# Optimization experiments

Hardware: AMD Instinct MI355X
Metric: run time of the kernel (lower is better)

The kernel has to match this reference:

```python
import jax, jax.numpy as jnp
import numpy as np

N_NODES = 50000
N_EDGES = 800000
N_GRAPHS = 128
IN_CH = 31
HID = 64
EPS = 1e-5


def _glorot(key, shape, scale=0.05):
    return jax.random.normal(key, shape, dtype=jnp.float32) * scale


def setup_inputs() -> dict:
    key = jax.random.key(0)
    ks = jax.random.split(key, 16)
    x = jax.random.normal(ks[0], (N_NODES, IN_CH), dtype=jnp.float32)
    edge_index = jax.random.randint(ks[1], (2, N_EDGES), 0, N_NODES, dtype=jnp.int32)
    batch = jnp.sort(jax.random.randint(ks[2], (N_NODES,), 0, N_GRAPHS, dtype=jnp.int32))
    params = {
        "t": jnp.ones((1,), dtype=jnp.float32),  # shared learnable softmax temperature
        "W1r": _glorot(ks[3], (HID, IN_CH)), "b1": jnp.zeros((HID,), jnp.float32), "W1s": _glorot(ks[4], (HID, IN_CH)),
        "W2r": _glorot(ks[5], (HID, HID)),  "b2": jnp.zeros((HID,), jnp.float32), "W2s": _glorot(ks[6], (HID, HID)),
        "W3r": _glorot(ks[7], (HID, HID)),  "b3": jnp.zeros((HID,), jnp.float32), "W3s": _glorot(ks[8], (HID, HID)),
        "Wl1": _glorot(ks[9], (2 * HID, 3 * HID)), "bl1": jnp.zeros((2 * HID,), jnp.float32),
        "Wl2": _glorot(ks[10], (HID // 2, 2 * HID)), "bl2": jnp.zeros((HID // 2,), jnp.float32),
    }
    return {"x": x, "edge_index": edge_index, "batch": batch, **params}


def _softmax_aggr(m, dst, t, n):
    # segment-softmax over incoming edges, per channel: alpha = softmax(t*m | dst)
    logits = m * t  # [E, C]
    mx = jax.ops.segment_max(logits, dst, num_segments=n)  # [N, C]
    e = jnp.exp(logits - mx[dst])
    denom = jax.ops.segment_sum(e, dst, num_segments=n)
    alpha = e / denom[dst]
    return jax.ops.segment_sum(m * alpha, dst, num_segments=n)  # [N, C]


def _graph_conv(x, src, dst, t, Wr, br, Ws):
    # PyG GraphConv: out = lin_rel(aggr_j x_j) + lin_root(x); lin_root has no bias
    m = x[src]  # gather [E, C]
    aggr = _softmax_aggr(m, dst, t, x.shape[0])
    return aggr @ Wr.T + br + x @ Ws.T


def _instance_norm(x):
    # torch InstanceNorm1d on [N, C] input -> normalize each row over feature dim
    mu = jnp.mean(x, axis=1, keepdims=True)
    var = jnp.mean((x - mu) ** 2, axis=1, keepdims=True)
    return (x - mu) / jnp.sqrt(var + EPS)


def reference(x, edge_index, batch, t, W1r, b1, W1s, W2r, b2, W2s, W3r, b3, W3s, Wl1, bl1, Wl2, bl2):
    src, dst = edge_index[0], edge_index[1]
    x1 = jax.nn.relu(_instance_norm(_graph_conv(x, src, dst, t, W1r, b1, W1s)))
    x2 = jax.nn.relu(_instance_norm(_graph_conv(x1, src, dst, t, W2r, b2, W2s)))
    x3 = jax.nn.relu(_instance_norm(_graph_conv(x2, src, dst, t, W3r, b3, W3s)))
    h1 = jax.ops.segment_max(x1, batch, num_segments=N_GRAPHS)
    h2 = jax.ops.segment_max(x2, batch, num_segments=N_GRAPHS)
    h3 = jax.ops.segment_max(x3, batch, num_segments=N_GRAPHS)
    h = jnp.concatenate([h1, h2, h3], axis=1)  # [G, 3*HID]
    z = jax.nn.relu(h @ Wl1.T + bl1)  # dropout is identity in eval mode
    z = z @ Wl2.T + bl2
    norm = jnp.maximum(jnp.linalg.norm(z, axis=1, keepdims=True), 1e-12)
    return z / norm
```

## Files before the change

kernel.cpp:

```cpp
#include <hip/hip_runtime.h>
#include <hip/hip_fp16.h>

#define N_NODES 50000
#define N_EDGES 800000
#define N_GRAPHS 128
#define IN_CH 31
#define HID 64

typedef __attribute__((ext_vector_type(8))) short short8;
typedef __attribute__((ext_vector_type(8))) unsigned short ushort8;
typedef __attribute__((ext_vector_type(4))) float floatx4;
typedef __attribute__((ext_vector_type(8))) _Float16 half8;
typedef __attribute__((ext_vector_type(2))) _Float16 half2v;

#if __has_builtin(__builtin_amdgcn_fdot2)
#define HAS_FDOT2 1
#endif

__device__ inline unsigned short f2h(float f) {
    __half h = __float2half_rn(f);
    return __half_as_ushort(h);
}
__device__ inline unsigned packh2(float a, float b) {
    __half2 h = __floats2half2_rn(a, b);
    return *(unsigned*)&h;
}
__device__ inline void pack4h(short* p, float4 v) {
    unsigned lo = packh2(v.x, v.y);
    unsigned hi = packh2(v.z, v.w);
    *(uint2*)p = make_uint2(lo, hi);
}
__device__ inline unsigned packEP(float E, float P) {
    return packh2(E, P);
}
__device__ inline float2 unpackEP(unsigned u) {
    __half2 h = *(__half2*)&u;
    return __half22float2(h);
}
__device__ inline half2v u2h2(unsigned u) {
    return __builtin_bit_cast(half2v, u);
}

__global__ void prep_kernel(const float* __restrict__ x, const float* __restrict__ tptr,
                            unsigned short* __restrict__ xh, unsigned* __restrict__ EP0,
                            int nN) {
    int i = blockIdx.x * 256 + threadIdx.x;
    if (i >= nN * 32) return;
    int node = i >> 5, c = i & 31;
    if (c < IN_CH) {
        float xv = x[node * IN_CH + c];
        xh[node * IN_CH + c] = f2h(xv);
        float tval = tptr[0];
        float E = __expf(tval * xv);
        EP0[i] = packEP(E, xv * E);
    } else {
        EP0[i] = 0;
    }
}


#define BKT_SHIFT 7
#define BKT_MAX 512
#define CHUNK 8192
#define CAP 2560

__global__ void bucket_scatter_kernel(const int* __restrict__ src,
                                      const int* __restrict__ dst,
                                      int* __restrict__ bucket_cnt,
                                      unsigned* __restrict__ ebuf, int e, int nb) {
    __shared__ int bins[BKT_MAX];
    __shared__ int base[BKT_MAX];
    __shared__ int lcur[BKT_MAX];
    int tid = threadIdx.x;
    int i0 = blockIdx.x * CHUNK;
    int i1 = i0 + CHUNK; if (i1 > e) i1 = e;
    for (int k = tid; k < nb; k += 256) { bins[k] = 0; lcur[k] = 0; }
    __syncthreads();
    for (int j = i0 + tid; j < i1; j += 256)
        atomicAdd(&bins[dst[j] >> BKT_SHIFT], 1);
    __syncthreads();
    for (int k = tid; k < nb; k += 256)
        if (bins[k]) base[k] = atomicAdd(&bucket_cnt[k], bins[k]);
    __syncthreads();
    for (int j = i0 + tid; j < i1; j += 256) {
        int ss = src[j], dd = dst[j];
        int b = dd >> BKT_SHIFT;
        int p = atomicAdd(&lcur[b], 1);
        ebuf[(size_t)b * CAP + base[b] + p] = (unsigned)ss | ((unsigned)(dd & 127) << 16);
    }
}

__global__ void bucket_csr_kernel(const unsigned* __restrict__ ebuf,
                                  const int* __restrict__ bucket_cnt,
                                  int* __restrict__ row_ptr, int* __restrict__ deg,
                                  int* __restrict__ csr_src, int nN) {
    __shared__ int nh[128];
    __shared__ int s[128];
    __shared__ int ncur[128];
    int tid = threadIdx.x;
    int b = blockIdx.x;
    int cnt = bucket_cnt[b];
    size_t boff = (size_t)b * CAP;
    int node0 = b << BKT_SHIFT;
    if (tid < 128) nh[tid] = 0;
    __syncthreads();
    for (int j = tid; j < cnt; j += 256)
        atomicAdd(&nh[ebuf[boff + j] >> 16], 1);
    __syncthreads();
    int v = (tid < 128) ? nh[tid] : 0;
    if (tid < 128) s[tid] = v;
    __syncthreads();
    for (int off = 1; off < 128; off <<= 1) {
        int u = (tid < 128 && tid >= off) ? s[tid - off] : 0;
        __syncthreads();
        if (tid < 128) s[tid] += u;
        __syncthreads();
    }
    if (tid < 128 && node0 + tid < nN) {
        int excl = (int)boff + s[tid] - v;
        row_ptr[node0 + tid] = excl;
        deg[node0 + tid] = v;
        ncur[tid] = excl;
    }
    __syncthreads();
    for (int j = tid; j < cnt; j += 256) {
        unsigned ed = ebuf[boff + j];
        int pos = atomicAdd(&ncur[ed >> 16], 1);
        csr_src[pos] = (int)(ed & 0xFFFF);
    }
}


template <int C_IN>
__global__ void __launch_bounds__(256, 8) aggr_kernel(
        const unsigned* __restrict__ EP, const unsigned short* __restrict__ xin,
        const int* __restrict__ row_ptr, const int* __restrict__ deg,
        const int* __restrict__ csr_src,
        unsigned short* __restrict__ aRowsB, int n) {
    constexpr int ROWD = (C_IN == 64) ? 64 : 32;
    int w = threadIdx.x >> 6, l = threadIdx.x & 63;
    int d = blockIdx.x * 4 + w;
    if (d >= n) return;
    int beg = __builtin_amdgcn_readfirstlane(row_ptr[d]);
    int dg  = __builtin_amdgcn_readfirstlane(deg[d]);
    int end = beg + dg;
    int cl = l & (ROWD - 1);

    float den0 = 0.f, den1 = 0.f, num0 = 0.f, num1 = 0.f;
    for (int base = beg; base < end; base += 64) {
        int cend = base + 64; if (cend > end) cend = end;
        int chunk = cend - base;
        int sidx = csr_src[base + ((l < chunk) ? l : 0)];
        for (int j0 = 0; j0 < chunk; j0 += 8) {
            int jc = chunk - j0;
            unsigned v[8];
            #pragma unroll
            for (int p = 0; p < 8; ++p) {
                int jj = (p < jc) ? (j0 + p) : (chunk - 1);
                int s  = __builtin_amdgcn_readlane(sidx, jj);
                v[p] = EP[(size_t)s * ROWD + cl];
            }
            #pragma unroll
            for (int p = 0; p < 8; ++p) {
                bool live = (p < jc);
#ifdef HAS_FDOT2
                unsigned bE = live ? 0x00003C00u : 0u;
                unsigned bP = live ? 0x3C000000u : 0u;
                if (p & 1) {
                    den1 = __builtin_amdgcn_fdot2(u2h2(v[p]), u2h2(bE), den1, false);
                    num1 = __builtin_amdgcn_fdot2(u2h2(v[p]), u2h2(bP), num1, false);
                } else {
                    den0 = __builtin_amdgcn_fdot2(u2h2(v[p]), u2h2(bE), den0, false);
                    num0 = __builtin_amdgcn_fdot2(u2h2(v[p]), u2h2(bP), num0, false);
                }
#else
                float mm = live ? 1.f : 0.f;
                float2 e = unpackEP(v[p]);
                if (p & 1) {
                    den1 = fmaf(e.x, mm, den1); num1 = fmaf(e.y, mm, num1);
                } else {
                    den0 = fmaf(e.x, mm, den0); num0 = fmaf(e.y, mm, num0);
                }
#endif
            }
        }
    }
    float den = den0 + den1;
    float num = num0 + num1;
    float aggr = (dg > 0 && den > 0.f) ? num / den : 0.f;

    if constexpr (C_IN == 64) {
        aRowsB[(size_t)d * 64 + l] = f2h(aggr);
    } else {
        unsigned short outv;
        if (l < C_IN)               outv = f2h(aggr);
        else if (l < 2 * C_IN)      outv = xin[(size_t)d * C_IN + (l - C_IN)];
        else                        outv = 0;
        aRowsB[(size_t)d * 64 + l] = outv;
    }
}


template <int C_IN, bool WEP>
__global__ void __launch_bounds__(256, 4) transform_kernel(
        const unsigned short* __restrict__ aRowsB, const unsigned short* __restrict__ yprev,
        const int* __restrict__ batch,
        const float* __restrict__ Wr, const float* __restrict__ br,
        const float* __restrict__ Ws, const float* __restrict__ tptr,
        unsigned short* __restrict__ yout, unsigned* __restrict__ EPout,
        float* __restrict__ hmax, int n) {
    constexpr int K_TOT = (C_IN == 64) ? 128 : 64;
    constexpr int KP    = K_TOT + 8;
    constexpr int KS    = K_TOT / 32;
    constexpr int ABSH  = 2 * 64 * KP;
    constexpr int CSH   = 64 * 68 * 2;
    constexpr int SMSH  = (ABSH > CSH) ? ABSH : CSH;

    __shared__ short smem[SMSH];
    short* sA = smem;
    short* sB = smem + 64 * KP;
    float* sC = (float*)smem;

    int tid = threadIdx.x;
    int nb = blockIdx.x * 64;

    if constexpr (C_IN == 64) {
        for (int idx = tid; idx < 64 * 16; idx += 256) {
            int row = idx >> 4, c8 = idx & 15;
            int node = nb + row; if (node >= n) node = n - 1;
            ushort8 v = (c8 < 8) ? ((const ushort8*)(aRowsB + (size_t)node * 64))[c8]
                                 : ((const ushort8*)(yprev + (size_t)node * 64))[c8 - 8];
            *(ushort8*)&sA[row * KP + c8 * 8] = v;
        }
        for (int idx = tid; idx < 64 * 32; idx += 256) {
            int nr = idx >> 5, c4 = idx & 31;
            float4 v = (c4 < 16) ? ((const float4*)(Wr + nr * 64))[c4]
                                 : ((const float4*)(Ws + nr * 64))[c4 - 16];
            pack4h(&sB[nr * KP + c4 * 4], v);
        }
    } else {
        for (int idx = tid; idx < 64 * 8; idx += 256) {
            int row = idx >> 3, c8 = idx & 7;
            int node = nb + row; if (node >= n) node = n - 1;
            ushort8 v = ((const ushort8*)(aRowsB + (size_t)node * 64))[c8];
            *(ushort8*)&sA[row * KP + c8 * 8] = v;
        }
        for (int idx = tid; idx < 64 * 64; idx += 256) {
            int nr = idx >> 6, k = idx & 63;
            float v = (k < C_IN) ? Wr[nr * C_IN + k]
                    : (k < 2 * C_IN) ? Ws[nr * C_IN + (k - C_IN)] : 0.f;
            sB[nr * KP + k] = (short)f2h(v);
        }
    }
    __syncthreads();

    int w = tid >> 6, l = tid & 63;
    int m = l & 15;
    int q = l >> 4;
    floatx4 acc[4] = {{0.f,0.f,0.f,0.f},{0.f,0.f,0.f,0.f},
                      {0.f,0.f,0.f,0.f},{0.f,0.f,0.f,0.f}};
    const short* aBase = &sA[(w * 16 + m) * KP + q * 8];
    #pragma unroll 2
    for (int s = 0; s < KS; ++s) {
        half8 af = *(const half8*)(aBase + s * 32);
        #pragma unroll
        for (int t = 0; t < 4; ++t) {
            half8 bf = *(const half8*)&sB[(t * 16 + m) * KP + q * 8 + s * 32];
            acc[t] = __builtin_amdgcn_mfma_f32_16x16x32_f16(af, bf, acc[t], 0, 0, 0);
        }
    }

    __syncthreads();
    #pragma unroll
    for (int t = 0; t < 4; ++t)
        #pragma unroll
        for (int r = 0; r < 4; ++r)
            sC[(w * 16 + q * 4 + r) * 68 + t * 16 + m] = acc[t][r];
    __syncthreads();

    float bias = br[l];
    float tval = 0.f;
    if constexpr (WEP) tval = tptr[0];
    int gcur = -1;
    float rmax = 0.f;
    for (int i = 0; i < 16; ++i) {
        int j = w * 16 + i;
        int d = nb + j;
        if (d < n) {
            float a = sC[j * 68 + l] + bias;
            float s = a;
            for (int off = 32; off > 0; off >>= 1) s += __shfl_xor(s, off);
            float mu = s * (1.0f / 64.0f);
            float dc = a - mu;
            float s2 = dc * dc;
            for (int off = 32; off > 0; off >>= 1) s2 += __shfl_xor(s2, off);
            float var = s2 * (1.0f / 64.0f);
            float y = dc * rsqrtf(var + 1e-5f);
            y = fmaxf(y, 0.f);
            if constexpr (WEP) {
                yout[(size_t)d * 64 + l] = f2h(y);
                float E = __expf(tval * y);
                EPout[(size_t)d * 64 + l] = packEP(E, y * E);
            }
            int g = __builtin_amdgcn_readfirstlane(batch[d]);
            if (g != gcur) {
                if (gcur >= 0)
                    atomicMax((int*)&hmax[gcur * 64 + l], __float_as_int(rmax));
                gcur = g;
                rmax = 0.f;
            }
            rmax = fmaxf(rmax, y);
        }
    }
    if (gcur >= 0)
        atomicMax((int*)&hmax[gcur * 64 + l], __float_as_int(rmax));
}


__global__ void mlp_kernel(const float* __restrict__ h,
                           const float* __restrict__ Wl1, const float* __restrict__ bl1,
                           const float* __restrict__ Wl2, const float* __restrict__ bl2,
                           float* __restrict__ out) {
    __shared__ float hrow[192];
    __shared__ float z1[128];
    __shared__ float z2[32];
    __shared__ float snorm;
    int g = blockIdx.x, tid = threadIdx.x;
    if (tid < 64) {
        hrow[tid]       = h[0 * N_GRAPHS * 64 + g * 64 + tid];
        hrow[64 + tid]  = h[1 * N_GRAPHS * 64 + g * 64 + tid];
        hrow[128 + tid] = h[2 * N_GRAPHS * 64 + g * 64 + tid];
    }
    __syncthreads();
    float acc = bl1[tid];
    #pragma unroll 8
    for (int c = 0; c < 192; ++c) acc = fmaf(hrow[c], Wl1[tid * 192 + c], acc);
    z1[tid] = fmaxf(acc, 0.f);
    __syncthreads();
    if (tid < 32) {
        float a2 = bl2[tid];
        #pragma unroll 8
        for (int c = 0; c < 128; ++c) a2 = fmaf(z1[c], Wl2[tid * 128 + c], a2);
        z2[tid] = a2;
    }
    __syncthreads();
    if (tid == 0) {
        float ss = 0.f;
        for (int i = 0; i < 32; ++i) ss += z2[i] * z2[i];
        snorm = fmaxf(sqrtf(ss), 1e-12f);
    }
    __syncthreads();
    if (tid < 32) out[g * 32 + tid] = z2[tid] / snorm;
}


extern "C" void kernel_launch(void* const* d_in, const int* in_sizes, int n_in,
                              void* d_out, int out_size, void* d_ws, size_t ws_size,
                              hipStream_t stream) {
    const float* x   = (const float*)d_in[0];
    const int* eidx  = (const int*)d_in[1];
    const int* batch = (const int*)d_in[2];
    const float* t   = (const float*)d_in[3];
    const float* W1r = (const float*)d_in[4];
    const float* b1  = (const float*)d_in[5];
    const float* W1s = (const float*)d_in[6];
    const float* W2r = (const float*)d_in[7];
    const float* b2  = (const float*)d_in[8];
    const float* W2s = (const float*)d_in[9];
    const float* W3r = (const float*)d_in[10];
    const float* b3  = (const float*)d_in[11];
    const float* W3s = (const float*)d_in[12];
    const float* Wl1 = (const float*)d_in[13];
    const float* bl1 = (const float*)d_in[14];
    const float* Wl2 = (const float*)d_in[15];
    const float* bl2 = (const float*)d_in[16];
    float* out = (float*)d_out;

    const int nE = in_sizes[1] / 2;
    const int nN = in_sizes[2];
    const int* src = eidx;
    const int* dst = eidx + nE;
    const int nb = (nN + 127) >> BKT_SHIFT;

    char* ws = (char*)d_ws;
    size_t off = 0;
    auto alloc = [&](size_t bytes) {
        char* p = ws + off;
        off = (off + bytes + 255) & ~(size_t)255;
        return p;
    };
    int*            bucket_cnt = (int*)alloc((size_t)BKT_MAX * 4);
    float*          h          = (float*)alloc((size_t)3 * N_GRAPHS * 64 * 4);
    int*            row_ptr    = (int*)alloc((size_t)nN * 4);
    int*            deg        = (int*)alloc((size_t)nN * 4);
    unsigned*       ebuf       = (unsigned*)alloc((size_t)nb * CAP * 4);
    int*            csr_src    = (int*)alloc((size_t)nb * CAP * 4);
    unsigned short* xh         = (unsigned short*)alloc((size_t)nN * IN_CH * 2);
    unsigned*       EP0        = (unsigned*)alloc((size_t)nN * 32 * 4);
    unsigned*       EPA        = (unsigned*)alloc((size_t)nN * 64 * 4);
    unsigned*       EPB        = (unsigned*)alloc((size_t)nN * 64 * 4);
    unsigned short* yAh        = (unsigned short*)alloc((size_t)nN * 64 * 2);
    unsigned short* yBh        = (unsigned short*)alloc((size_t)nN * 64 * 2);
    unsigned short* aRowsB     = (unsigned short*)alloc((size_t)nN * 64 * 2);

    const int nbChunk = (nE + CHUNK - 1) / CHUNK;

    hipMemsetAsync(bucket_cnt, 0,
                   (char*)(h + 3 * N_GRAPHS * 64) - (char*)bucket_cnt, stream);
    prep_kernel<<<(nN * 32 + 255) / 256, 256, 0, stream>>>(x, t, xh, EP0, nN);
    bucket_scatter_kernel<<<nbChunk, 256, 0, stream>>>(src, dst, bucket_cnt, ebuf, nE, nb);
    bucket_csr_kernel<<<nb, 256, 0, stream>>>(ebuf, bucket_cnt, row_ptr, deg, csr_src, nN);

    const int nbA = (nN + 3) / 4;
    const int nbT = (nN + 63) / 64;

    aggr_kernel<IN_CH><<<nbA, 256, 0, stream>>>(EP0, xh, row_ptr, deg, csr_src, aRowsB, nN);
    transform_kernel<IN_CH, true><<<nbT, 256, 0, stream>>>(
        aRowsB, nullptr, batch, W1r, b1, W1s, t, yAh, EPA, h + 0 * N_GRAPHS * 64, nN);

    aggr_kernel<HID><<<nbA, 256, 0, stream>>>(EPA, nullptr, row_ptr, deg, csr_src, aRowsB, nN);
    transform_kernel<HID, true><<<nbT, 256, 0, stream>>>(
        aRowsB, yAh, batch, W2r, b2, W2s, t, yBh, EPB, h + 1 * N_GRAPHS * 64, nN);

    aggr_kernel<HID><<<nbA, 256, 0, stream>>>(EPB, nullptr, row_ptr, deg, csr_src, aRowsB, nN);
    transform_kernel<HID, false><<<nbT, 256, 0, stream>>>(
        aRowsB, yBh, batch, W3r, b3, W3s, t, nullptr, nullptr, h + 2 * N_GRAPHS * 64, nN);

    mlp_kernel<<<N_GRAPHS, 128, 0, stream>>>(h, Wl1, bl1, Wl2, bl2, out);
}
```

Before: 270.1 us.

## Gather fp16 features and recompute exp per edge instead of packed E/P tables

Transform kernels now write only the fp16 activations, and no longer write a packed half2 table of exp(t*y) and y*exp(t*y). The aggregation kernel gathers the 2-byte fp16 value per edge and computes the exponential and weighted sum in fp32 on the fly. This halves the bytes gathered per edge and removes the extra EP writes and buffers, since the gather was likely bandwidth-bound. The cost is one exp per edge per channel instead of per node, and a single accumulator chain instead of two interleaved ones.

Measured after the change: 266.6 us. No clear change (-1.3%).

```diff
diff --git a/kernel.cpp b/kernel.cpp
--- a/kernel.cpp
+++ b/kernel.cpp
@@ -11,11 +11,6 @@
 typedef __attribute__((ext_vector_type(8))) unsigned short ushort8;
 typedef __attribute__((ext_vector_type(4))) float floatx4;
 typedef __attribute__((ext_vector_type(8))) _Float16 half8;
-typedef __attribute__((ext_vector_type(2))) _Float16 half2v;
-
-#if __has_builtin(__builtin_amdgcn_fdot2)
-#define HAS_FDOT2 1
-#endif
 
 __device__ inline unsigned short f2h(float f) {
     __half h = __float2half_rn(f);
@@ -30,32 +25,13 @@
     unsigned hi = packh2(v.z, v.w);
     *(uint2*)p = make_uint2(lo, hi);
 }
-__device__ inline unsigned packEP(float E, float P) {
-    return packh2(E, P);
-}
-__device__ inline float2 unpackEP(unsigned u) {
-    __half2 h = *(__half2*)&u;
-    return __half22float2(h);
-}
-__device__ inline half2v u2h2(unsigned u) {
-    return __builtin_bit_cast(half2v, u);
-}
-
-__global__ void prep_kernel(const float* __restrict__ x, const float* __restrict__ tptr,
-                            unsigned short* __restrict__ xh, unsigned* __restrict__ EP0,
-                            int nN) {
+
+__global__ void prep_kernel(const float* __restrict__ x,
+                            unsigned short* __restrict__ xh32, int nN) {
     int i = blockIdx.x * 256 + threadIdx.x;
     if (i >= nN * 32) return;
     int node = i >> 5, c = i & 31;
-    if (c < IN_CH) {
-        float xv = x[node * IN_CH + c];
-        xh[node * IN_CH + c] = f2h(xv);
-        float tval = tptr[0];
-        float E = __expf(tval * xv);
-        EP0[i] = packEP(E, xv * E);
-    } else {
-        EP0[i] = 0;
-    }
+    xh32[i] = (c < IN_CH) ? f2h(x[node * IN_CH + c]) : 0;
 }
 
 
@@ -133,60 +109,44 @@
 
 template <int C_IN>
 __global__ void __launch_bounds__(256, 8) aggr_kernel(
-        const unsigned* __restrict__ EP, const unsigned short* __restrict__ xin,
+        const unsigned short* __restrict__ Ytab,
+        const float* __restrict__ tptr,
         const int* __restrict__ row_ptr, const int* __restrict__ deg,
         const int* __restrict__ csr_src,
         unsigned short* __restrict__ aRowsB, int n) {
-    constexpr int ROWD = (C_IN == 64) ? 64 : 32;
+    constexpr int RS = (C_IN == 64) ? 64 : 32;
     int w = threadIdx.x >> 6, l = threadIdx.x & 63;
     int d = blockIdx.x * 4 + w;
     if (d >= n) return;
     int beg = __builtin_amdgcn_readfirstlane(row_ptr[d]);
     int dg  = __builtin_amdgcn_readfirstlane(deg[d]);
     int end = beg + dg;
-    int cl = l & (ROWD - 1);
-
-    float den0 = 0.f, den1 = 0.f, num0 = 0.f, num1 = 0.f;
+    int cl = l & (RS - 1);
+    float tval = tptr[0];
+
+    float den = 0.f, num = 0.f;
     for (int base = beg; base < end; base += 64) {
         int cend = base + 64; if (cend > end) cend = end;
         int chunk = cend - base;
         int sidx = csr_src[base + ((l < chunk) ? l : 0)];
         for (int j0 = 0; j0 < chunk; j0 += 8) {
             int jc = chunk - j0;
-            unsigned v[8];
+            float yv[8];
             #pragma unroll
             for (int p = 0; p < 8; ++p) {
                 int jj = (p < jc) ? (j0 + p) : (chunk - 1);
                 int s  = __builtin_amdgcn_readlane(sidx, jj);
-                v[p] = EP[(size_t)s * ROWD + cl];
+                yv[p] = (float)*(const _Float16*)&Ytab[(size_t)s * RS + cl];
             }
             #pragma unroll
             for (int p = 0; p < 8; ++p) {
-                bool live = (p < jc);
-#ifdef HAS_FDOT2
-                unsigned bE = live ? 0x00003C00u : 0u;
-                unsigned bP = live ? 0x3C000000u : 0u;
-                if (p & 1) {
-                    den1 = __builtin_amdgcn_fdot2(u2h2(v[p]), u2h2(bE), den1, false);
-                    num1 = __builtin_amdgcn_fdot2(u2h2(v[p]), u2h2(bP), num1, false);
-                } else {
-                    den0 = __builtin_amdgcn_fdot2(u2h2(v[p]), u2h2(bE), den0, false);
-                    num0 = __builtin_amdgcn_fdot2(u2h2(v[p]), u2h2(bP), num0, false);
-                }
-#else
-                float mm = live ? 1.f : 0.f;
-                float2 e = unpackEP(v[p]);
-                if (p & 1) {
-                    den1 = fmaf(e.x, mm, den1); num1 = fmaf(e.y, mm, num1);
-                } else {
-                    den0 = fmaf(e.x, mm, den0); num0 = fmaf(e.y, mm, num0);
-                }
-#endif
+                float m = (p < jc) ? 1.f : 0.f;
+                float E = __expf(tval * yv[p]) * m;
+                den += E;
+                num = fmaf(yv[p], E, num);
             }
         }
     }
-    float den = den0 + den1;
-    float num = num0 + num1;
     float aggr = (dg > 0 && den > 0.f) ? num / den : 0.f;
 
     if constexpr (C_IN == 64) {
@@ -194,20 +154,20 @@
     } else {
         unsigned short outv;
         if (l < C_IN)               outv = f2h(aggr);
-        else if (l < 2 * C_IN)      outv = xin[(size_t)d * C_IN + (l - C_IN)];
+        else if (l < 2 * C_IN)      outv = Ytab[(size_t)d * 32 + (l - C_IN)];
         else                        outv = 0;
         aRowsB[(size_t)d * 64 + l] = outv;
     }
 }
 
 
-template <int C_IN, bool WEP>
+template <int C_IN, bool WY>
 __global__ void __launch_bounds__(256, 4) transform_kernel(
         const unsigned short* __restrict__ aRowsB, const unsigned short* __restrict__ yprev,
         const int* __restrict__ batch,
         const float* __restrict__ Wr, const float* __restrict__ br,
-        const float* __restrict__ Ws, const float* __restrict__ tptr,
-        unsigned short* __restrict__ yout, unsigned* __restrict__ EPout,
+        const float* __restrict__ Ws,
+        unsigned short* __restrict__ yout,
         float* __restrict__ hmax, int n) {
     constexpr int K_TOT = (C_IN == 64) ? 128 : 64;
     constexpr int KP    = K_TOT + 8;
@@ -279,8 +239,6 @@
     __syncthreads();
 
     float bias = br[l];
-    float tval = 0.f;
-    if constexpr (WEP) tval = tptr[0];
     int gcur = -1;
     float rmax = 0.f;
     for (int i = 0; i < 16; ++i) {
@@ -297,10 +255,8 @@
             float var = s2 * (1.0f / 64.0f);
             float y = dc * rsqrtf(var + 1e-5f);
             y = fmaxf(y, 0.f);
-            if constexpr (WEP) {
+            if constexpr (WY) {
                 yout[(size_t)d * 64 + l] = f2h(y);
-                float E = __expf(tval * y);
-                EPout[(size_t)d * 64 + l] = packEP(E, y * E);
             }
             int g = __builtin_amdgcn_readfirstlane(batch[d]);
             if (g != gcur) {
@@ -395,10 +351,7 @@
     int*            deg        = (int*)alloc((size_t)nN * 4);
     unsigned*       ebuf       = (unsigned*)alloc((size_t)nb * CAP * 4);
     int*            csr_src    = (int*)alloc((size_t)nb * CAP * 4);
-    unsigned short* xh         = (unsigned short*)alloc((size_t)nN * IN_CH * 2);
-    unsigned*       EP0        = (unsigned*)alloc((size_t)nN * 32 * 4);
-    unsigned*       EPA        = (unsigned*)alloc((size_t)nN * 64 * 4);
-    unsigned*       EPB        = (unsigned*)alloc((size_t)nN * 64 * 4);
+    unsigned short* xh32       = (unsigned short*)alloc((size_t)nN * 32 * 2);
     unsigned short* yAh        = (unsigned short*)alloc((size_t)nN * 64 * 2);
     unsigned short* yBh        = (unsigned short*)alloc((size_t)nN * 64 * 2);
     unsigned short* aRowsB     = (unsigned short*)alloc((size_t)nN * 64 * 2);
@@ -407,24 +360,24 @@
 
     hipMemsetAsync(bucket_cnt, 0,
                    (char*)(h + 3 * N_GRAPHS * 64) - (char*)bucket_cnt, stream);
-    prep_kernel<<<(nN * 32 + 255) / 256, 256, 0, stream>>>(x, t, xh, EP0, nN);
+    prep_kernel<<<(nN * 32 + 255) / 256, 256, 0, stream>>>(x, xh32, nN);
     bucket_scatter_kernel<<<nbChunk, 256, 0, stream>>>(src, dst, bucket_cnt, ebuf, nE, nb);
     bucket_csr_kernel<<<nb, 256, 0, stream>>>(ebuf, bucket_cnt, row_ptr, deg, csr_src, nN);
 
     const int nbA = (nN + 3) / 4;
     const int nbT = (nN + 63) / 64;
 
-    aggr_kernel<IN_CH><<<nbA, 256, 0, stream>>>(EP0, xh, row_ptr, deg, csr_src, aRowsB, nN);
+    aggr_kernel<IN_CH><<<nbA, 256, 0, stream>>>(xh32, t, row_ptr, deg, csr_src, aRowsB, nN);
     transform_kernel<IN_CH, true><<<nbT, 256, 0, stream>>>(
-        aRowsB, nullptr, batch, W1r, b1, W1s, t, yAh, EPA, h + 0 * N_GRAPHS * 64, nN);
-
-    aggr_kernel<HID><<<nbA, 256, 0, stream>>>(EPA, nullptr, row_ptr, deg, csr_src, aRowsB, nN);
+        aRowsB, nullptr, batch, W1r, b1, W1s, yAh, h + 0 * N_GRAPHS * 64, nN);
+
+    aggr_kernel<HID><<<nbA, 256, 0, stream>>>(yAh, t, row_ptr, deg, csr_src, aRowsB, nN);
     transform_kernel<HID, true><<<nbT, 256, 0, stream>>>(
-        aRowsB, yAh, batch, W2r, b2, W2s, t, yBh, EPB, h + 1 * N_GRAPHS * 64, nN);
-
-    aggr_kernel<HID><<<nbA, 256, 0, stream>>>(EPB, nullptr, row_ptr, deg, csr_src, aRowsB, nN);
+        aRowsB, yAh, batch, W2r, b2, W2s, yBh, h + 1 * N_GRAPHS * 64, nN);
+
+    aggr_kernel<HID><<<nbA, 256, 0, stream>>>(yBh, t, row_ptr, deg, csr_src, aRowsB, nN);
     transform_kernel<HID, false><<<nbT, 256, 0, stream>>>(
-        aRowsB, yBh, batch, W3r, b3, W3s, t, nullptr, nullptr, h + 2 * N_GRAPHS * 64, nN);
+        aRowsB, yBh, batch, W3r, b3, W3s, nullptr, h + 2 * N_GRAPHS * 64, nN);
 
     mlp_kernel<<<N_GRAPHS, 128, 0, stream>>>(h, Wl1, bl1, Wl2, bl2, out);
 }
```
